# Performance work log

Measured on AMD Instinct MI355X. Metric: run time of the kernel, lower is better.

The kernel has to match this reference:

```python
import jax, jax.numpy as jnp
import numpy as np

N_HEAD = 12
N_TILES = 10  # forward hardcodes t = T // 10 and repeats the tril mask 10x10


def setup_inputs() -> dict:
    key = jax.random.key(0)
    ks = jax.random.split(key, 9)
    B, T, C = 2, 2560, 768
    s = 1.0 / np.sqrt(C)
    x = jax.random.normal(ks[0], (B, T, C), dtype=jnp.float32)
    Wk = jax.random.normal(ks[1], (C, C), dtype=jnp.float32) * s
    bk = jnp.zeros((C,), dtype=jnp.float32)
    Wq = jax.random.normal(ks[2], (C, C), dtype=jnp.float32) * s
    bq = jnp.zeros((C,), dtype=jnp.float32)
    Wv = jax.random.normal(ks[3], (C, C), dtype=jnp.float32) * s
    bv = jnp.zeros((C,), dtype=jnp.float32)
    Wp = jax.random.normal(ks[4], (C, C), dtype=jnp.float32) * s
    bp = jnp.zeros((C,), dtype=jnp.float32)
    return {"x": x, "Wk": Wk, "bk": bk, "Wq": Wq, "bq": bq,
            "Wv": Wv, "bv": bv, "Wp": Wp, "bp": bp}


def reference(x, Wk, bk, Wq, bq, Wv, bv, Wp, bp):
    B, T, C = x.shape
    hd = C // N_HEAD
    t = T // N_TILES
    # linear projections (torch nn.Linear: x @ W.T + b)
    k = (x @ Wk.T + bk).reshape(B, T, N_HEAD, hd).transpose(0, 2, 1, 3)  # [B,H,T,hd]
    q = (x @ Wq.T + bq).reshape(B, T, N_HEAD, hd).transpose(0, 2, 1, 3)
    v = (x @ Wv.T + bv).reshape(B, T, N_HEAD, hd).transpose(0, 2, 1, 3)
    att = jnp.einsum('bhqd,bhkd->bhqk', q, k) * (1.0 / np.sqrt(hd))  # [B,H,T,T]
    # repeated block-tril mask: tril(t,t) tiled 10x10 over TxT
    idx = jnp.arange(T)
    mask = (idx[:, None] % t) >= (idx[None, :] % t)  # [T,T] bool
    att = jnp.where(mask[None, None], att, -jnp.inf)
    att = jax.nn.softmax(att, axis=-1)
    y = jnp.einsum('bhqk,bhkd->bhqd', att, v)  # [B,H,T,hd]
    y = y.transpose(0, 2, 1, 3).reshape(B, T, C)
    return y @ Wp.T + bp
```

## Files before the change

### kernel.cpp

```cpp
#include <hip/hip_runtime.h>

typedef unsigned short u16;
typedef unsigned int u32;
typedef __bf16 bf16x8 __attribute__((ext_vector_type(8)));
typedef short s16x4 __attribute__((ext_vector_type(4)));
typedef float f32x4 __attribute__((ext_vector_type(4)));

#define CC 768
#define TT 2560
#define NH 12
#define HD 64
#define KDIM 768

#define QSCALE 0.18033688011112042f

__device__ __forceinline__ u16 f2bf(float f) {
  u32 u = __builtin_bit_cast(u32, f);
  u32 r = u + 0x7fffu + ((u >> 16) & 1u);
  return (u16)(r >> 16);
}

#if __has_builtin(__builtin_amdgcn_mfma_f32_16x16x16bf16_1k)
__device__ __forceinline__ f32x4 mfma16b(s16x4 a, s16x4 b, f32x4 c) {
  return __builtin_amdgcn_mfma_f32_16x16x16bf16_1k(a, b, c, 0, 0, 0);
}
#else
__device__ __forceinline__ f32x4 mfma16b(s16x4 a, s16x4 b, f32x4 c) {
  f32x4 d;
  asm("v_mfma_f32_16x16x16_bf16 %0, %1, %2, %3\n\ts_nop 7\n\ts_nop 7"
      : "=v"(d) : "v"(a), "v"(b), "v"(c));
  return d;
}
#endif

__global__ void convall(const float* __restrict__ x,
                        const float* __restrict__ Wq, const float* __restrict__ Wk,
                        const float* __restrict__ Wv, const float* __restrict__ Wp,
                        u16* __restrict__ xb, u16* __restrict__ wqb, u16* __restrict__ wkb,
                        u16* __restrict__ wvb, u16* __restrict__ wpb,
                        int nx4, int nw4) {
  int z = blockIdx.y;
  const float* in; u16* out; int n4;
  switch (z) {
    case 0: in = x;  out = xb;  n4 = nx4; break;
    case 1: in = Wq; out = wqb; n4 = nw4; break;
    case 2: in = Wk; out = wkb; n4 = nw4; break;
    case 3: in = Wv; out = wvb; n4 = nw4; break;
    default: in = Wp; out = wpb; n4 = nw4; break;
  }
  int i = blockIdx.x * blockDim.x + threadIdx.x;
  if (i >= n4) return;
  float4 v = ((const float4*)in)[i];
  ushort4 o;
  o.x = f2bf(v.x); o.y = f2bf(v.y); o.z = f2bf(v.z); o.w = f2bf(v.w);
  ((ushort4*)out)[i] = o;
}

__global__ __launch_bounds__(256) void gemm_qkv(
    const u16* __restrict__ xb,
    const u16* __restrict__ wqb, const u16* __restrict__ wkb, const u16* __restrict__ wvb,
    const float* __restrict__ bq, const float* __restrict__ bk, const float* __restrict__ bv,
    u16* __restrict__ qo, u16* __restrict__ ko, u16* __restrict__ vo)
{
  __shared__ __align__(16) u16 lds_a[128 * 72];
  __shared__ __align__(16) u16 lds_b[128 * 72];
  int z = blockIdx.z;
  const u16* W = (z == 0) ? wqb : (z == 1 ? wkb : wvb);
  const float* bias = (z == 0) ? bq : (z == 1 ? bk : bv);
  int n0 = blockIdx.x * 128;
  int m0 = blockIdx.y * 128;
  int tid = threadIdx.x;
  int lane = tid & 63, wv_ = tid >> 6;
  int wm = wv_ & 1, wn = wv_ >> 1;
  int mcol = lane & 15, quad = lane >> 4;
  int chunk = tid & 7, rbase = tid >> 3;

  f32x4 acc[4][4] = {};

  for (int k0 = 0; k0 < KDIM; k0 += 64) {
    __syncthreads();
#pragma unroll
    for (int r = 0; r < 4; ++r) {
      int row = rbase + r * 32;
      *(uint4*)&lds_a[row * 72 + chunk * 8] =
          *(const uint4*)&xb[(size_t)(m0 + row) * KDIM + k0 + chunk * 8];
      *(uint4*)&lds_b[row * 72 + chunk * 8] =
          *(const uint4*)&W[(size_t)(n0 + row) * KDIM + k0 + chunk * 8];
    }
    __syncthreads();
#pragma unroll
    for (int kc = 0; kc < 2; ++kc) {
      bf16x8 af[4], bfr[4];
#pragma unroll
      for (int i = 0; i < 4; i++)
        af[i] = *(const bf16x8*)&lds_a[(wm * 64 + i * 16 + mcol) * 72 + kc * 32 + quad * 8];
#pragma unroll
      for (int i = 0; i < 4; i++)
        bfr[i] = *(const bf16x8*)&lds_b[(wn * 64 + i * 16 + mcol) * 72 + kc * 32 + quad * 8];
#pragma unroll
      for (int i = 0; i < 4; i++)
#pragma unroll
        for (int j = 0; j < 4; j++)
          acc[i][j] = __builtin_amdgcn_mfma_f32_16x16x32_bf16(af[i], bfr[j], acc[i][j], 0, 0, 0);
    }
  }

#pragma unroll
  for (int i = 0; i < 4; i++) {
    int rowb = m0 + wm * 64 + i * 16 + quad * 4;
    int b = rowb / TT;
    int tt0 = rowb - b * TT;
#pragma unroll
    for (int j = 0; j < 4; j++) {
      int col = n0 + wn * 64 + j * 16 + mcol;
      int h = col >> 6, d = col & 63;
      float bb_ = bias[col];
      size_t bhoff = (size_t)(b * NH + h) * (TT * HD);
      if (z == 2) {
        ushort4 pk;
        pk.x = f2bf(acc[i][j][0] + bb_);
        pk.y = f2bf(acc[i][j][1] + bb_);
        pk.z = f2bf(acc[i][j][2] + bb_);
        pk.w = f2bf(acc[i][j][3] + bb_);
        *(ushort4*)&vo[bhoff + (size_t)(tt0 >> 4) * 1024 + d * 16 + (tt0 & 15)] = pk;
      } else if (z == 1) {
        size_t base = bhoff + (size_t)(tt0 >> 4) * 1024 + (d >> 5) * 512 + (d & 31);
#pragma unroll
        for (int r = 0; r < 4; r++)
          ko[base + ((tt0 & 15) + r) * 32] = f2bf(acc[i][j][r] + bb_);
      } else {
#pragma unroll
        for (int r = 0; r < 4; r++)
          qo[bhoff + (size_t)(tt0 + r) * HD + d] = f2bf((acc[i][j][r] + bb_) * QSCALE);
      }
    }
  }
}

struct Strip {
  bf16x8 qf0, qf1;
  f32x4 o0, o1, o2, o3;
  f32x4 racc;
};

__device__ __forceinline__ void strip_step(
    Strip& S, bf16x8 kf0, bf16x8 kf1,
    s16x4 vf0, s16x4 vf1, s16x4 vf2, s16x4 vf3,
    bool maskg, int mcol, int quad)
{
  f32x4 st = {0.f, 0.f, 0.f, 0.f};
  st = __builtin_amdgcn_mfma_f32_16x16x32_bf16(kf0, S.qf0, st, 0, 0, 0);
  st = __builtin_amdgcn_mfma_f32_16x16x32_bf16(kf1, S.qf1, st, 0, 0, 0);
  float p0 = __builtin_amdgcn_exp2f(st[0]);
  float p1 = __builtin_amdgcn_exp2f(st[1]);
  float p2 = __builtin_amdgcn_exp2f(st[2]);
  float p3 = __builtin_amdgcn_exp2f(st[3]);
  if (maskg) {
    int j0 = quad * 4;
    p0 = (j0 + 0 > mcol) ? 0.f : p0;
    p1 = (j0 + 1 > mcol) ? 0.f : p1;
    p2 = (j0 + 2 > mcol) ? 0.f : p2;
    p3 = (j0 + 3 > mcol) ? 0.f : p3;
  }
  u32 b0 = __builtin_bit_cast(u32, p0) + 0x8000u;
  u32 b1 = __builtin_bit_cast(u32, p1) + 0x8000u;
  u32 b2 = __builtin_bit_cast(u32, p2) + 0x8000u;
  u32 b3 = __builtin_bit_cast(u32, p3) + 0x8000u;
  uint2 pk;
  pk.x = __builtin_amdgcn_perm(b1, b0, 0x07060302u);
  pk.y = __builtin_amdgcn_perm(b3, b2, 0x07060302u);
  s16x4 pf = __builtin_bit_cast(s16x4, pk);
  const s16x4 ones = {0x3F80, 0x3F80, 0x3F80, 0x3F80};
  S.racc = mfma16b(ones, pf, S.racc);
  S.o0 = mfma16b(vf0, pf, S.o0);
  S.o1 = mfma16b(vf1, pf, S.o1);
  S.o2 = mfma16b(vf2, pf, S.o2);
  S.o3 = mfma16b(vf3, pf, S.o3);
}

__global__ __launch_bounds__(64) void attn(
    const u16* __restrict__ q, const u16* __restrict__ kg,
    const u16* __restrict__ vg, u16* __restrict__ y)
{
  int lane = threadIdx.x & 63;
  int mcol = lane & 15, quad = lane >> 4;
  int gid = blockIdx.x;
  int c = gid & 7;
  int idx = gid >> 3;
  int sub = idx / 40;
  int s = idx - sub * 40;
  int bh = c * 3 + sub;
  int hb = s >> 3;
  int r = s & 7;
  int b = bh / NH, h = bh - b * NH;
  const u16* qp = q + (size_t)bh * TT * HD;
  const u16* kp = kg + (size_t)bh * TT * HD;
  const u16* vp = vg + (size_t)bh * TT * HD;

  int base = hb * 512;
  int rh = 7 - r;
  int qr[4];
  qr[0] = base + r * 16;
  qr[1] = base + 128 + rh * 16;
  qr[2] = base + 256 + r * 16;
  qr[3] = base + 384 + rh * 16;

  Strip S[4];
#pragma unroll
  for (int i = 0; i < 4; ++i) {
    S[i].qf0 = *(const bf16x8*)&qp[(size_t)(qr[i] + mcol) * HD + quad * 8];
    S[i].qf1 = *(const bf16x8*)&qp[(size_t)(qr[i] + mcol) * HD + 32 + quad * 8];
    S[i].o0 = {0.f, 0.f, 0.f, 0.f};
    S[i].o1 = {0.f, 0.f, 0.f, 0.f};
    S[i].o2 = {0.f, 0.f, 0.f, 0.f};
    S[i].o3 = {0.f, 0.f, 0.f, 0.f};
    S[i].racc = {0.f, 0.f, 0.f, 0.f};
  }

  int koff = mcol * 32 + quad * 8;
  int voff = mcol * 16 + quad * 4;

  for (int kt = 0; kt < 20; ++kt) {
    const u16* ktb = kp + kt * (128 * HD);
    const u16* vtb = vp + kt * (128 * HD);
    if ((kt & 1) == 0) {
#pragma unroll
      for (int g = 0; g < 8; ++g) {
        bf16x8 kf0 = *(const bf16x8*)&ktb[g * 1024 + koff];
        bf16x8 kf1 = *(const bf16x8*)&ktb[g * 1024 + 512 + koff];
        s16x4 vf0 = *(const s16x4*)&vtb[g * 1024 + 0 * 256 + voff];
        s16x4 vf1 = *(const s16x4*)&vtb[g * 1024 + 1 * 256 + voff];
        s16x4 vf2 = *(const s16x4*)&vtb[g * 1024 + 2 * 256 + voff];
        s16x4 vf3 = *(const s16x4*)&vtb[g * 1024 + 3 * 256 + voff];
        strip_step(S[1], kf0, kf1, vf0, vf1, vf2, vf3, false, mcol, quad);
        strip_step(S[3], kf0, kf1, vf0, vf1, vf2, vf3, false, mcol, quad);
        if (g <= r) {
          bool mg = (g == r);
          strip_step(S[0], kf0, kf1, vf0, vf1, vf2, vf3, mg, mcol, quad);
          strip_step(S[2], kf0, kf1, vf0, vf1, vf2, vf3, mg, mcol, quad);
        }
      }
    } else {
      for (int g = 0; g <= rh; ++g) {
        bf16x8 kf0 = *(const bf16x8*)&ktb[g * 1024 + koff];
        bf16x8 kf1 = *(const bf16x8*)&ktb[g * 1024 + 512 + koff];
        s16x4 vf0 = *(const s16x4*)&vtb[g * 1024 + 0 * 256 + voff];
        s16x4 vf1 = *(const s16x4*)&vtb[g * 1024 + 1 * 256 + voff];
        s16x4 vf2 = *(const s16x4*)&vtb[g * 1024 + 2 * 256 + voff];
        s16x4 vf3 = *(const s16x4*)&vtb[g * 1024 + 3 * 256 + voff];
        bool mg = (g == rh);
        strip_step(S[1], kf0, kf1, vf0, vf1, vf2, vf3, mg, mcol, quad);
        strip_step(S[3], kf0, kf1, vf0, vf1, vf2, vf3, mg, mcol, quad);
      }
    }
  }

#pragma unroll
  for (int i = 0; i < 4; ++i) {
    float inv = 1.0f / S[i].racc[0];
    size_t yrow = ((size_t)(b * TT + qr[i] + mcol)) * CC + h * HD;
    f32x4 oo[4] = {S[i].o0, S[i].o1, S[i].o2, S[i].o3};
#pragma unroll
    for (int df = 0; df < 4; ++df) {
      ushort4 pk;
      pk.x = f2bf(oo[df][0] * inv);
      pk.y = f2bf(oo[df][1] * inv);
      pk.z = f2bf(oo[df][2] * inv);
      pk.w = f2bf(oo[df][3] * inv);
      *(ushort4*)&y[yrow + df * 16 + quad * 4] = pk;
    }
  }
}

__global__ __launch_bounds__(256) void gemm_out(
    const u16* __restrict__ yb, const u16* __restrict__ wpb,
    const float* __restrict__ bp, float* __restrict__ out)
{
  __shared__ __align__(16) u16 lds_a[128 * 72];
  __shared__ __align__(16) u16 lds_b[128 * 72];
  int n0 = blockIdx.x * 128;
  int m0 = blockIdx.y * 128;
  int tid = threadIdx.x;
  int lane = tid & 63, wv_ = tid >> 6;
  int wm = wv_ & 1, wn = wv_ >> 1;
  int mcol = lane & 15, quad = lane >> 4;
  int chunk = tid & 7, rbase = tid >> 3;

  f32x4 acc[4][4] = {};

  for (int k0 = 0; k0 < KDIM; k0 += 64) {
    __syncthreads();
#pragma unroll
    for (int r = 0; r < 4; ++r) {
      int row = rbase + r * 32;
      *(uint4*)&lds_a[row * 72 + chunk * 8] =
          *(const uint4*)&yb[(size_t)(m0 + row) * KDIM + k0 + chunk * 8];
      *(uint4*)&lds_b[row * 72 + chunk * 8] =
          *(const uint4*)&wpb[(size_t)(n0 + row) * KDIM + k0 + chunk * 8];
    }
    __syncthreads();
#pragma unroll
    for (int kc = 0; kc < 2; ++kc) {
      bf16x8 af[4], bfr[4];
#pragma unroll
      for (int i = 0; i < 4; i++)
        af[i] = *(const bf16x8*)&lds_a[(wm * 64 + i * 16 + mcol) * 72 + kc * 32 + quad * 8];
#pragma unroll
      for (int i = 0; i < 4; i++)
        bfr[i] = *(const bf16x8*)&lds_b[(wn * 64 + i * 16 + mcol) * 72 + kc * 32 + quad * 8];
#pragma unroll
      for (int i = 0; i < 4; i++)
#pragma unroll
        for (int j = 0; j < 4; j++)
          acc[i][j] = __builtin_amdgcn_mfma_f32_16x16x32_bf16(af[i], bfr[j], acc[i][j], 0, 0, 0);
    }
  }

#pragma unroll
  for (int i = 0; i < 4; i++) {
    int row0 = m0 + wm * 64 + i * 16 + quad * 4;
#pragma unroll
    for (int j = 0; j < 4; j++) {
      int col = n0 + wn * 64 + j * 16 + mcol;
      float bb_ = bp[col];
#pragma unroll
      for (int r = 0; r < 4; r++)
        out[(size_t)(row0 + r) * CC + col] = acc[i][j][r] + bb_;
    }
  }
}

extern "C" void kernel_launch(void* const* d_in, const int* in_sizes, int n_in,
                              void* d_out, int out_size, void* d_ws, size_t ws_size,
                              hipStream_t stream) {
  const float* x  = (const float*)d_in[0];
  const float* Wk = (const float*)d_in[1];
  const float* bk = (const float*)d_in[2];
  const float* Wq = (const float*)d_in[3];
  const float* bq = (const float*)d_in[4];
  const float* Wv = (const float*)d_in[5];
  const float* bv = (const float*)d_in[6];
  const float* Wp = (const float*)d_in[7];
  const float* bp = (const float*)d_in[8];
  float* out = (float*)d_out;

  char* ws = (char*)d_ws;
  size_t off = 0;
  auto alloc = [&](size_t bytes) {
    void* p = ws + off;
    off += (bytes + 255) & ~(size_t)255;
    return p;
  };
  const size_t NX = (size_t)2 * TT * CC;
  const size_t NW = (size_t)CC * CC;
  u16* xb  = (u16*)alloc(NX * 2);
  u16* wqb = (u16*)alloc(NW * 2);
  u16* wkb = (u16*)alloc(NW * 2);
  u16* wvb = (u16*)alloc(NW * 2);
  u16* wpb = (u16*)alloc(NW * 2);
  u16* qws = (u16*)alloc(NX * 2);
  u16* kws = (u16*)alloc(NX * 2);
  u16* vgw = (u16*)alloc(NX * 2);
  u16* yws = (u16*)alloc(NX * 2);

  int nx4 = (int)(NX / 4), nw4 = (int)(NW / 4);
  convall<<<dim3((nx4 + 255) / 256, 5), 256, 0, stream>>>(
      x, Wq, Wk, Wv, Wp, xb, wqb, wkb, wvb, wpb, nx4, nw4);

  gemm_qkv<<<dim3(6, 40, 3), 256, 0, stream>>>(xb, wqb, wkb, wvb, bq, bk, bv,
                                               qws, kws, vgw);
  attn<<<dim3(960), 64, 0, stream>>>(qws, kws, vgw, yws);
  gemm_out<<<dim3(6, 40), 256, 0, stream>>>(yws, wpb, bp, out);
}
```

Baseline: 218.3 us.

## Split attention key loop across two waves with LDS reduction

Each attention block now runs two wavefronts, each covering half of the key tiles, instead of one wavefront covering all of them. The second wave writes its partial output accumulators and row sums to shared memory, and the first wave adds them before normalising and storing. This doubles the number of active waves so the GPU is better occupied, in exchange for shared-memory traffic, a block barrier and higher LDS usage per block.

```diff
diff --git a/kernel.cpp b/kernel.cpp
--- a/kernel.cpp
+++ b/kernel.cpp
@@ -178,11 +178,17 @@
   S.o3 = mfma16b(vf3, pf, S.o3);
 }
 
-__global__ __launch_bounds__(64) void attn(
+#define OSTR 68
+
+__global__ __launch_bounds__(128) void attn(
     const u16* __restrict__ q, const u16* __restrict__ kg,
     const u16* __restrict__ vg, u16* __restrict__ y)
 {
-  int lane = threadIdx.x & 63;
+  __shared__ float lds_o[4][16 * OSTR];
+  __shared__ float lds_r[64];
+
+  int tid = threadIdx.x;
+  int lane = tid & 63, w = tid >> 6;
   int mcol = lane & 15, quad = lane >> 4;
   int gid = blockIdx.x;
   int c = gid & 7;
@@ -220,7 +226,7 @@
   int koff = mcol * 32 + quad * 8;
   int voff = mcol * 16 + quad * 4;
 
-  for (int kt = 0; kt < 20; ++kt) {
+  for (int kt = w * 10; kt < w * 10 + 10; ++kt) {
     const u16* ktb = kp + kt * (128 * HD);
     const u16* vtb = vp + kt * (128 * HD);
     if ((kt & 1) == 0) {
@@ -255,19 +261,34 @@
     }
   }
 
-#pragma unroll
-  for (int i = 0; i < 4; ++i) {
-    float inv = 1.0f / S[i].racc[0];
-    size_t yrow = ((size_t)(b * TT + qr[i] + mcol)) * CC + h * HD;
-    f32x4 oo[4] = {S[i].o0, S[i].o1, S[i].o2, S[i].o3};
-#pragma unroll
-    for (int df = 0; df < 4; ++df) {
-      ushort4 pk;
-      pk.x = f2bf(oo[df][0] * inv);
-      pk.y = f2bf(oo[df][1] * inv);
-      pk.z = f2bf(oo[df][2] * inv);
-      pk.w = f2bf(oo[df][3] * inv);
-      *(ushort4*)&y[yrow + df * 16 + quad * 4] = pk;
+  if (w == 1) {
+#pragma unroll
+    for (int i = 0; i < 4; ++i) {
+      f32x4 oo[4] = {S[i].o0, S[i].o1, S[i].o2, S[i].o3};
+#pragma unroll
+      for (int df = 0; df < 4; ++df)
+        *(f32x4*)&lds_o[i][mcol * OSTR + df * 16 + quad * 4] = oo[df];
+      if (quad == 0) lds_r[i * 16 + mcol] = S[i].racc[0];
+    }
+  }
+  __syncthreads();
+  if (w == 0) {
+#pragma unroll
+    for (int i = 0; i < 4; ++i) {
+      float denom = S[i].racc[0] + lds_r[i * 16 + mcol];
+      float inv = 1.0f / denom;
+      f32x4 oo[4] = {S[i].o0, S[i].o1, S[i].o2, S[i].o3};
+      size_t yrow = ((size_t)(b * TT + qr[i] + mcol)) * CC + h * HD;
+#pragma unroll
+      for (int df = 0; df < 4; ++df) {
+        f32x4 other = *(const f32x4*)&lds_o[i][mcol * OSTR + df * 16 + quad * 4];
+        ushort4 pk;
+        pk.x = f2bf((oo[df][0] + other[0]) * inv);
+        pk.y = f2bf((oo[df][1] + other[1]) * inv);
+        pk.z = f2bf((oo[df][2] + other[2]) * inv);
+        pk.w = f2bf((oo[df][3] + other[3]) * inv);
+        *(ushort4*)&y[yrow + df * 16 + quad * 4] = pk;
+      }
     }
   }
 }
@@ -369,6 +390,6 @@
 
   gemm_qkv<<<dim3(6, 40, 3), 256, 0, stream>>>(xb, wqb, wkb, wvb, bq, bk, bv,
                                                qws, kws, vgw);
-  attn<<<dim3(960), 64, 0, stream>>>(qws, kws, vgw, yws);
+  attn<<<dim3(960), 128, 0, stream>>>(qws, kws, vgw, yws);
   gemm_out<<<dim3(6, 40), 256, 0, stream>>>(yws, wpb, bp, out);
 }
```

After: 193.4 us. 1.13x faster.
